# Kernel optimization log

Measured on AMD Instinct MI355X. Metric: run time of the kernel, lower is better.

## Reference

```python
import jax, jax.numpy as jnp
import numpy as np

NUM_HEADS = 12


def _rope(t, cos, sin):
    # t: (B, H, M, D); cos/sin: (M, D//2) applied to interleaved pairs
    B, H, M, D = t.shape
    t2 = t.reshape(B, H, M, D // 2, 2)
    t0, t1 = t2[..., 0], t2[..., 1]
    c = cos[None, None]  # (1,1,M,D//2)
    s = sin[None, None]
    r0 = t0 * c - t1 * s
    r1 = t0 * s + t1 * c
    return jnp.stack([r0, r1], axis=-1).reshape(B, H, M, D)


def setup_inputs() -> dict:
    key = jax.random.key(0)
    ks = jax.random.split(key, 7)
    B, N, C = 16, 577, 768
    Hd = C // NUM_HEADS
    x = jax.random.normal(ks[0], (B, N, C), dtype=jnp.float32)
    # rotary angles for N-1 non-CLS tokens
    theta = jax.random.uniform(ks[1], (N - 1, Hd // 2), dtype=jnp.float32) * 6.28318
    cos = jnp.cos(theta)
    sin = jnp.sin(theta)
    w_qkv = jax.random.normal(ks[2], (C, 3 * C), dtype=jnp.float32) * 0.02
    b_qkv = jax.random.normal(ks[3], (3 * C,), dtype=jnp.float32) * 0.02
    w_proj = jax.random.normal(ks[4], (C, C), dtype=jnp.float32) * 0.02
    b_proj = jax.random.normal(ks[5], (C,), dtype=jnp.float32) * 0.02
    return {"x": x, "cos": cos, "sin": sin, "w_qkv": w_qkv, "b_qkv": b_qkv,
            "w_proj": w_proj, "b_proj": b_proj}


def reference(x, cos, sin, w_qkv, b_qkv, w_proj, b_proj):
    B, N, C = x.shape
    H = NUM_HEADS
    D = C // H
    scale = D ** -0.5
    qkv = x @ w_qkv + b_qkv                       # (B, N, 3C)
    qkv = qkv.reshape(B, N, 3, H, D).transpose(2, 0, 3, 1, 4)  # (3, B, H, N, D)
    q, k, v = qkv[0], qkv[1], qkv[2]
    # RoPE applied to all tokens except the CLS token (index 0)
    q = jnp.concatenate([q[:, :, :1], _rope(q[:, :, 1:], cos, sin)], axis=2)
    k = jnp.concatenate([k[:, :, :1], _rope(k[:, :, 1:], cos, sin)], axis=2)
    attn = jax.nn.softmax(jnp.einsum('bhnd,bhmd->bhnm', q, k) * scale, axis=-1)
    out = jnp.einsum('bhnm,bhmd->bhnd', attn, v)  # (B, H, N, D)
    out = out.transpose(0, 2, 1, 3).reshape(B, N, C)
    return out @ w_proj + b_proj
```

## Files before the change

kernel.cpp:

```cpp
#include <hip/hip_runtime.h>
#include <stdint.h>

typedef unsigned short u16;
typedef __attribute__((ext_vector_type(8))) short bf16x8;
typedef __attribute__((ext_vector_type(4))) float f32x4;

#define MFMA16(a, b, c) __builtin_amdgcn_mfma_f32_16x16x32_bf16((a), (b), (c), 0, 0, 0)

__device__ __forceinline__ float b2f(u16 u) {
    union { unsigned int i; float f; } v; v.i = ((unsigned int)u) << 16; return v.f;
}
__device__ __forceinline__ u16 f2b(float f) {
    union { float f; unsigned int i; } v; v.f = f;
    unsigned int r = v.i + 0x7fffu + ((v.i >> 16) & 1u);
    return (u16)(r >> 16);
}
__device__ __forceinline__ float exp2_fast(float x) {
    float r; __asm__("v_exp_f32 %0, %1" : "=v"(r) : "v"(x)); return r;
}

typedef __attribute__((address_space(1))) void gvoid;
typedef __attribute__((address_space(3))) void lvoid;
__device__ __forceinline__ void gld16(const void* g, void* l) {
    __builtin_amdgcn_global_load_lds((gvoid*)(void*)g, (lvoid*)l, 16, 0, 0);
}

__device__ __forceinline__ void tile_from_bid(int bid, int nTM, int nTN,
                                              int& rt, int& ct) {
    const int PW = 8;
    const int full = nTM / PW;
    const int per = PW * nTN;
    int p = bid / per;
    int pw = PW;
    int rem = bid - p * per;
    if (p >= full) { p = full; rem = bid - full * per; pw = nTM - full * PW; }
    const int c = rem / pw;
    const int r = rem - c * pw;
    rt = p * PW + r;
    ct = c;
}

__global__ __launch_bounds__(256) void prep(const float* __restrict__ x,
                                            u16* __restrict__ xb,
                                            const float* __restrict__ wqkv,
                                            const float* __restrict__ wproj,
                                            u16* __restrict__ outQ,
                                            u16* __restrict__ outP) {
    __shared__ float tile[32][33];
    const int t = threadIdx.x;
    int bid = blockIdx.x;
    if (bid < 6924) {
        const int i = (bid * 256 + t) * 4;
        if (i + 3 < 7090176) {
            const float4 v = *(const float4*)(x + i);
            ushort4 o;
            o.x = f2b(v.x); o.y = f2b(v.y); o.z = f2b(v.z); o.w = f2b(v.w);
            *(ushort4*)(xb + i) = o;
        }
        return;
    }
    bid -= 6924;
    int bx = bid % 96;
    const int by = bid / 96;
    const float* in; u16* out; int C;
    if (bx < 72) { in = wqkv; out = outQ; C = 2304; }
    else         { bx -= 72; in = wproj; out = outP; C = 768; }
    const int R = 768;
    const int r = t >> 3, c4 = (t & 7) * 4;
    const int ir = by * 32 + r, ic = bx * 32 + c4;
    const float4 v = *(const float4*)(in + (size_t)ir * C + ic);
    tile[r][c4 + 0] = v.x; tile[r][c4 + 1] = v.y;
    tile[r][c4 + 2] = v.z; tile[r][c4 + 3] = v.w;
    __syncthreads();
    const int orow = bx * 32 + r, ocol = by * 32 + c4;
    ushort4 o;
    o.x = f2b(tile[c4 + 0][r]); o.y = f2b(tile[c4 + 1][r]);
    o.z = f2b(tile[c4 + 2][r]); o.w = f2b(tile[c4 + 3][r]);
    *(ushort4*)(out + (size_t)orow * R + ocol) = o;
}

template <int EPI>
__global__ __launch_bounds__(512) void gemm_bt(const u16* __restrict__ A,
                                               const u16* __restrict__ Bt,
                                               const float* __restrict__ bias,
                                               void* __restrict__ Cv,
                                               const float* __restrict__ cosp,
                                               const float* __restrict__ sinp,
                                               u16* __restrict__ VtG,
                                               int M, int N, int K) {
    __shared__ __align__(16) u16 As0[128 * 64];
    __shared__ __align__(16) u16 As1[128 * 64];
    __shared__ __align__(16) u16 Bs0[128 * 64];
    __shared__ __align__(16) u16 Bs1[128 * 64];

    const int t = threadIdx.x;
    const int lane = t & 63;
    const int wave = t >> 6;
    const int l15 = lane & 15, quad = lane >> 4;
    const int wm = wave >> 2;
    const int wn = wave & 3;

    int rt, ct;
    tile_from_bid(blockIdx.y * gridDim.x + blockIdx.x, gridDim.x, gridDim.y, rt, ct);
    const int row0 = rt * 128;
    const int col0 = ct * 128;

    const f32x4 fz = {0.f, 0.f, 0.f, 0.f};
    f32x4 acc[4][2];
#pragma unroll
    for (int i = 0; i < 4; ++i)
#pragma unroll
        for (int j = 0; j < 2; ++j) acc[i][j] = fz;

    const u16* Ap[2];
    const u16* Bp[2];
    int off[2];
#pragma unroll
    for (int n = 0; n < 2; ++n) {
        const int g = t + n * 512;
        const int row = g >> 3;
        const int slot = (g & 7) ^ (row & 7);
        int ar = row0 + row; if (ar > M - 1) ar = M - 1;
        Ap[n] = A + (size_t)ar * K + slot * 8;
        Bp[n] = Bt + (size_t)(col0 + row) * K + slot * 8;
        off[n] = g * 8;
    }

#define STAGE(kt_, Ad, Bd) do {                                            \
        const int kb_ = (kt_) << 6;                                        \
        gld16(Ap[0] + kb_, (Ad) + off[0]);                                 \
        gld16(Ap[1] + kb_, (Ad) + off[1]);                                 \
        gld16(Bp[0] + kb_, (Bd) + off[0]);                                 \
        gld16(Bp[1] + kb_, (Bd) + off[1]);                                 \
    } while (0)

#define COMPUTE(Asb, Bsb) do {                                             \
        _Pragma("unroll")                                                  \
        for (int kk = 0; kk < 2; ++kk) {                                   \
            const int swk = ((kk * 4 + quad) ^ (l15 & 7)) * 8;             \
            bf16x8 af[4], bfr[2];                                          \
            _Pragma("unroll")                                              \
            for (int mi = 0; mi < 4; ++mi)                                 \
                af[mi] = *(const bf16x8*)((Asb) +                          \
                    ((wm * 4 + mi) * 16 + l15) * 64 + swk);                \
            _Pragma("unroll")                                              \
            for (int ni = 0; ni < 2; ++ni)                                 \
                bfr[ni] = *(const bf16x8*)((Bsb) +                         \
                    ((wn * 2 + ni) * 16 + l15) * 64 + swk);                \
            _Pragma("unroll")                                              \
            for (int mi = 0; mi < 4; ++mi)                                 \
                _Pragma("unroll")                                          \
                for (int ni = 0; ni < 2; ++ni)                             \
                    acc[mi][ni] = MFMA16(bfr[ni], af[mi], acc[mi][ni]);    \
        }                                                                  \
    } while (0)

    const int nKT = K >> 6;
    STAGE(0, As0, Bs0);
    __syncthreads();

    for (int kt = 0; kt < nKT; kt += 2) {
        if (kt + 1 < nKT) STAGE(kt + 1, As1, Bs1);
        COMPUTE(As0, Bs0);
        __syncthreads();
        if (kt + 2 < nKT) STAGE(kt + 2, As0, Bs0);
        COMPUTE(As1, Bs1);
        __syncthreads();
    }
#undef STAGE
#undef COMPUTE

    if (EPI == 2) {
        if (col0 >= 1536) {
#pragma unroll
            for (int mi = 0; mi < 4; ++mi) {
                const int row = row0 + wm * 64 + mi * 16 + l15;
                if (row < M) {
                    const int bb = row / 577, n = row - bb * 577;
                    u16* vdst = VtG + (size_t)bb * 491520 + n;
#pragma unroll
                    for (int ni = 0; ni < 2; ++ni) {
                        const int colb = col0 + wn * 32 + ni * 16 + quad * 4;
                        const float4 bv = *(const float4*)(bias + colb);
#pragma unroll
                        for (int r = 0; r < 4; ++r) {
                            const int cv = colb + r - 1536;
                            vdst[(size_t)(cv >> 6) * 40960 + (cv & 63) * 640] =
                                f2b(acc[mi][ni][r] + ((const float*)&bv)[r]);
                        }
                    }
                }
            }
        } else {
#pragma unroll
            for (int mi = 0; mi < 4; ++mi) {
                const int row = row0 + wm * 64 + mi * 16 + l15;
                if (row < M) {
                    const int bb = row / 577, n = row - bb * 577;
                    const bool hr = (n >= 1);
                    const float* cb = cosp + (size_t)(hr ? (n - 1) : 0) * 32;
                    const float* sb = sinp + (size_t)(hr ? (n - 1) : 0) * 32;
                    u16* outp = (u16*)Cv + (size_t)row * 1536;
#pragma unroll
                    for (int ni = 0; ni < 2; ++ni) {
                        const int colb = col0 + wn * 32 + ni * 16 + quad * 4;
                        const float4 bv = *(const float4*)(bias + colb);
                        const int pi = (colb & 63) >> 1;
                        float2 c = *(const float2*)(cb + pi);
                        float2 s = *(const float2*)(sb + pi);
                        if (!hr) { c.x = 1.f; c.y = 1.f; s.x = 0.f; s.y = 0.f; }
                        const float v0 = acc[mi][ni][0] + bv.x;
                        const float v1 = acc[mi][ni][1] + bv.y;
                        const float v2 = acc[mi][ni][2] + bv.z;
                        const float v3 = acc[mi][ni][3] + bv.w;
                        ushort4 o;
                        o.x = f2b(v0 * c.x - v1 * s.x);
                        o.y = f2b(v0 * s.x + v1 * c.x);
                        o.z = f2b(v2 * c.y - v3 * s.y);
                        o.w = f2b(v2 * s.y + v3 * c.y);
                        *(ushort4*)(outp + colb) = o;
                    }
                }
            }
        }
    } else {
#pragma unroll
        for (int ni = 0; ni < 2; ++ni) {
            const int colb = col0 + wn * 32 + ni * 16 + quad * 4;
            const float4 bv = *(const float4*)(bias + colb);
#pragma unroll
            for (int mi = 0; mi < 4; ++mi) {
                const int row = row0 + wm * 64 + mi * 16 + l15;
                if (row < M) {
                    float4 o;
                    o.x = acc[mi][ni][0] + bv.x; o.y = acc[mi][ni][1] + bv.y;
                    o.z = acc[mi][ni][2] + bv.z; o.w = acc[mi][ni][3] + bv.w;
                    *(float4*)((float*)Cv + (size_t)row * N + colb) = o;
                }
            }
        }
    }
}

#define PSTR 72
#define CEXP 0.18033688011112042f

__global__ __launch_bounds__(512, 8) void attn2(const u16* __restrict__ qkv,
                                                const u16* __restrict__ VtG,
                                                u16* __restrict__ aout) {
    __shared__ __align__(16) u16 Ks[64 * 64];
    __shared__ __align__(16) u16 Vs[64 * 64];
    __shared__ __align__(16) u16 Pb[8 * 16 * PSTR];

    const int t = threadIdx.x;
    const int lane = t & 63, wave = t >> 6;
    const int l15 = lane & 15, quad = lane >> 4;

    const int bid = blockIdx.x;
    const int swz = (bid & 7) * 120 + (bid >> 3);
    const int bh = swz / 5, qt = swz - bh * 5;
    const int b = bh / 12, h = bh - b * 12;
    const u16* baseQ = qkv + (size_t)b * 577 * 1536 + h * 64;
    const u16* baseK = baseQ + 768;
    const u16* vbase = VtG + (size_t)bh * 64 * 640;

    const int mq = qt * 128 + wave * 16 + l15;
    const int nq = mq < 577 ? mq : 576;
    bf16x8 aq[2];
    aq[0] = *(const bf16x8*)(baseQ + (size_t)nq * 1536 + quad * 8);
    aq[1] = *(const bf16x8*)(baseQ + (size_t)nq * 1536 + 32 + quad * 8);

    const int r0 = t >> 3;
    const int s0 = (t & 7) ^ (r0 & 7);
    const int o0 = t * 8;
    const u16* Kp = baseK + (size_t)r0 * 1536 + s0 * 8;
    const u16* Vp = vbase + (size_t)r0 * 640 + s0 * 8;

    const int swk0 = (quad ^ (l15 & 7)) * 8;
    const int swk1 = ((4 + quad) ^ (l15 & 7)) * 8;

    u16* Pw = Pb + wave * 16 * PSTR;

    f32x4 oacc[4];
    const f32x4 fz = {0.f, 0.f, 0.f, 0.f};
#pragma unroll
    for (int i = 0; i < 4; ++i) oacc[i] = fz;
    float m1 = -1e30f;
    float l1 = 0.f;

#define ATT_TILE(kt_, MASKED) do {                                          \
        f32x4 sacc[4];                                                      \
        _Pragma("unroll")                                                   \
        for (int nt = 0; nt < 4; ++nt) {                                    \
            sacc[nt] = fz;                                                  \
            const bf16x8 bk0 = *(const bf16x8*)(Ks + (nt * 16 + l15) * 64 + swk0); \
            sacc[nt] = MFMA16(bk0, aq[0], sacc[nt]);                        \
            const bf16x8 bk1 = *(const bf16x8*)(Ks + (nt * 16 + l15) * 64 + swk1); \
            sacc[nt] = MFMA16(bk1, aq[1], sacc[nt]);                        \
        }                                                                   \
        if (MASKED) {                                                       \
            _Pragma("unroll")                                               \
            for (int nt = 0; nt < 4; ++nt)                                  \
                _Pragma("unroll")                                           \
                for (int r = 0; r < 4; ++r)                                 \
                    if (nt * 16 + quad * 4 + r > 0) sacc[nt][r] = -1e30f;   \
        }                                                                   \
        float mA = fmaxf(fmaxf(sacc[0][0], sacc[0][1]), fmaxf(sacc[0][2], sacc[0][3])); \
        float mB = fmaxf(fmaxf(sacc[1][0], sacc[1][1]), fmaxf(sacc[1][2], sacc[1][3])); \
        float mC = fmaxf(fmaxf(sacc[2][0], sacc[2][1]), fmaxf(sacc[2][2], sacc[2][3])); \
        float mD = fmaxf(fmaxf(sacc[3][0], sacc[3][1]), fmaxf(sacc[3][2], sacc[3][3])); \
        float mt = fmaxf(fmaxf(mA, mB), fmaxf(mC, mD));                     \
        mt = fmaxf(mt, __shfl_xor(mt, 16));                                 \
        mt = fmaxf(mt, __shfl_xor(mt, 32));                                 \
        const float mnew = fmaxf(m1, mt);                                   \
        const float alpha = exp2_fast((m1 - mnew) * CEXP);                  \
        m1 = mnew;                                                          \
        const float nmc = -mnew * CEXP;                                     \
        float lsum = 0.f;                                                   \
        _Pragma("unroll")                                                   \
        for (int nt = 0; nt < 4; ++nt) {                                    \
            const float p0 = exp2_fast(__builtin_fmaf(sacc[nt][0], CEXP, nmc)); \
            const float p1 = exp2_fast(__builtin_fmaf(sacc[nt][1], CEXP, nmc)); \
            const float p2 = exp2_fast(__builtin_fmaf(sacc[nt][2], CEXP, nmc)); \
            const float p3 = exp2_fast(__builtin_fmaf(sacc[nt][3], CEXP, nmc)); \
            lsum += (p0 + p1) + (p2 + p3);                                  \
            ushort4 pk;                                                     \
            pk.x = f2b(p0); pk.y = f2b(p1); pk.z = f2b(p2); pk.w = f2b(p3); \
            *(ushort4*)(Pw + l15 * PSTR + nt * 16 + quad * 4) = pk;         \
        }                                                                   \
        _Pragma("unroll")                                                   \
        for (int dt = 0; dt < 4; ++dt) {                                    \
            oacc[dt][0] *= alpha; oacc[dt][1] *= alpha;                     \
            oacc[dt][2] *= alpha; oacc[dt][3] *= alpha;                     \
        }                                                                   \
        __asm__ __volatile__("s_waitcnt lgkmcnt(0)" ::: "memory");          \
        _Pragma("unroll")                                                   \
        for (int kc = 0; kc < 2; ++kc) {                                    \
            const bf16x8 pf = *(const bf16x8*)(Pw + l15 * PSTR + kc * 32 + quad * 8); \
            const int swkv = kc ? swk1 : swk0;                              \
            _Pragma("unroll")                                               \
            for (int dt = 0; dt < 4; ++dt) {                                \
                const bf16x8 vf = *(const bf16x8*)(Vs + (dt * 16 + l15) * 64 + swkv); \
                oacc[dt] = MFMA16(vf, pf, oacc[dt]);                        \
            }                                                               \
        }                                                                   \
        lsum += __shfl_xor(lsum, 16);                                       \
        lsum += __shfl_xor(lsum, 32);                                       \
        l1 = l1 * alpha + lsum;                                             \
    } while (0)

    for (int kt = 0; kt < 9; ++kt) {
        gld16(Kp + (size_t)kt * 98304, Ks + o0);
        gld16(Vp + kt * 64, Vs + o0);
        __syncthreads();
        ATT_TILE(kt, false);
        __syncthreads();
    }
    gld16(baseK + (size_t)576 * 1536 + s0 * 8, Ks + o0);
    gld16(Vp + 576, Vs + o0);
    __syncthreads();
    ATT_TILE(9, true);

#undef ATT_TILE

    const int n = qt * 128 + wave * 16 + l15;
    if (n < 577) {
        const float linv = 1.f / l1;
        u16* op = aout + ((size_t)b * 577 + n) * 768 + h * 64 + quad * 4;
#pragma unroll
        for (int dt = 0; dt < 4; ++dt) {
            ushort4 o;
            o.x = f2b(oacc[dt][0] * linv); o.y = f2b(oacc[dt][1] * linv);
            o.z = f2b(oacc[dt][2] * linv); o.w = f2b(oacc[dt][3] * linv);
            *(ushort4*)(op + dt * 16) = o;
        }
    }
}

extern "C" void kernel_launch(void* const* d_in, const int* in_sizes, int n_in,
                              void* d_out, int out_size, void* d_ws, size_t ws_size,
                              hipStream_t stream) {
    const float* x      = (const float*)d_in[0];
    const float* cosp   = (const float*)d_in[1];
    const float* sinp   = (const float*)d_in[2];
    const float* w_qkv  = (const float*)d_in[3];
    const float* b_qkv  = (const float*)d_in[4];
    const float* w_proj = (const float*)d_in[5];
    const float* b_proj = (const float*)d_in[6];
    float* out = (float*)d_out;

    char* ws = (char*)d_ws;
    u16* xb     = (u16*)(ws);
    u16* aout   = (u16*)(ws);
    u16* wqkvT  = (u16*)(ws + 14180352);
    u16* wprojT = (u16*)(ws + 17719296);
    u16* qkv    = (u16*)(ws + 18898944);
    u16* VtG    = (u16*)(ws + 47259648);

    prep<<<9228, 256, 0, stream>>>(x, xb, w_qkv, w_proj, wqkvT, wprojT);
    gemm_bt<2><<<dim3(73, 18), 512, 0, stream>>>(xb, wqkvT, b_qkv, qkv,
                                                 cosp, sinp, VtG, 9232, 2304, 768);
    attn2<<<dim3(960), 512, 0, stream>>>(qkv, VtG, aout);
    gemm_bt<1><<<dim3(73, 6), 512, 0, stream>>>(aout, wprojT, b_proj, out,
                                                nullptr, nullptr, nullptr, 9232, 768, 768);
}
```

Before: 212.5 us.

## Use 256x128 single-buffered tile for QKV GEMM with fused RoPE/V-transpose epilogue

Splits the templated GEMM into a dedicated QKV kernel with a 256x128 block tile, a 4x4 MFMA fragment per wave (2x4 wave grid), and a simple single-buffered LDS loop. The grouped tile-ordering width becomes a parameter, set to 4 for the QKV GEMM. The goal is more arithmetic per LDS load and fewer blocks (666 instead of 1314), cutting global and LDS traffic for the largest GEMM. The cost is losing the double-buffered load/compute overlap, higher register pressure from 16 accumulators, and fewer blocks to spread across the CUs.

```diff
diff --git a/kernel.cpp b/kernel.cpp
--- a/kernel.cpp
+++ b/kernel.cpp
@@ -25,9 +25,8 @@
     __builtin_amdgcn_global_load_lds((gvoid*)(void*)g, (lvoid*)l, 16, 0, 0);
 }
 
-__device__ __forceinline__ void tile_from_bid(int bid, int nTM, int nTN,
+__device__ __forceinline__ void tile_from_bid(int bid, int nTM, int nTN, int PW,
                                               int& rt, int& ct) {
-    const int PW = 8;
     const int full = nTM / PW;
     const int per = PW * nTN;
     int p = bid / per;
@@ -79,15 +78,144 @@
     *(ushort4*)(out + (size_t)orow * R + ocol) = o;
 }
 
-template <int EPI>
-__global__ __launch_bounds__(512) void gemm_bt(const u16* __restrict__ A,
-                                               const u16* __restrict__ Bt,
-                                               const float* __restrict__ bias,
-                                               void* __restrict__ Cv,
-                                               const float* __restrict__ cosp,
-                                               const float* __restrict__ sinp,
-                                               u16* __restrict__ VtG,
-                                               int M, int N, int K) {
+__global__ __launch_bounds__(512) void gemm1k(const u16* __restrict__ A,
+                                              const u16* __restrict__ Bt,
+                                              const float* __restrict__ bias,
+                                              u16* __restrict__ qkv,
+                                              const float* __restrict__ cosp,
+                                              const float* __restrict__ sinp,
+                                              u16* __restrict__ VtG,
+                                              int M, int N, int K) {
+    __shared__ __align__(16) u16 As[256 * 64];
+    __shared__ __align__(16) u16 Bs[128 * 64];
+
+    const int t = threadIdx.x;
+    const int lane = t & 63;
+    const int wave = t >> 6;
+    const int l15 = lane & 15, quad = lane >> 4;
+    const int wm = wave >> 1;
+    const int wn = wave & 1;
+
+    int rt, ct;
+    tile_from_bid(blockIdx.y * gridDim.x + blockIdx.x, gridDim.x, gridDim.y, 4, rt, ct);
+    const int row0 = rt * 256;
+    const int col0 = ct * 128;
+
+    const f32x4 fz = {0.f, 0.f, 0.f, 0.f};
+    f32x4 acc[4][4];
+#pragma unroll
+    for (int i = 0; i < 4; ++i)
+#pragma unroll
+        for (int j = 0; j < 4; ++j) acc[i][j] = fz;
+
+    const u16* Ap[4]; int offA[4];
+    const u16* Bp[2]; int offB[2];
+#pragma unroll
+    for (int n = 0; n < 4; ++n) {
+        const int g = t + n * 512;
+        const int row = g >> 3;
+        const int slot = (g & 7) ^ (row & 7);
+        int ar = row0 + row; if (ar > M - 1) ar = M - 1;
+        Ap[n] = A + (size_t)ar * K + slot * 8;
+        offA[n] = g * 8;
+    }
+#pragma unroll
+    for (int n = 0; n < 2; ++n) {
+        const int g = t + n * 512;
+        const int row = g >> 3;
+        const int slot = (g & 7) ^ (row & 7);
+        Bp[n] = Bt + (size_t)(col0 + row) * K + slot * 8;
+        offB[n] = g * 8;
+    }
+
+    const int nKT = K >> 6;
+    for (int kt = 0; kt < nKT; ++kt) {
+        const int kb = kt << 6;
+        gld16(Ap[0] + kb, As + offA[0]);
+        gld16(Ap[1] + kb, As + offA[1]);
+        gld16(Ap[2] + kb, As + offA[2]);
+        gld16(Ap[3] + kb, As + offA[3]);
+        gld16(Bp[0] + kb, Bs + offB[0]);
+        gld16(Bp[1] + kb, Bs + offB[1]);
+        __syncthreads();
+#pragma unroll
+        for (int kk = 0; kk < 2; ++kk) {
+            const int swk = ((kk * 4 + quad) ^ (l15 & 7)) * 8;
+            bf16x8 af[4], bfr[4];
+#pragma unroll
+            for (int mi = 0; mi < 4; ++mi)
+                af[mi] = *(const bf16x8*)(As + ((wm * 4 + mi) * 16 + l15) * 64 + swk);
+#pragma unroll
+            for (int ni = 0; ni < 4; ++ni)
+                bfr[ni] = *(const bf16x8*)(Bs + ((wn * 4 + ni) * 16 + l15) * 64 + swk);
+#pragma unroll
+            for (int mi = 0; mi < 4; ++mi)
+#pragma unroll
+                for (int ni = 0; ni < 4; ++ni)
+                    acc[mi][ni] = MFMA16(bfr[ni], af[mi], acc[mi][ni]);
+        }
+        __syncthreads();
+    }
+
+    if (col0 >= 1536) {
+#pragma unroll
+        for (int mi = 0; mi < 4; ++mi) {
+            const int row = row0 + wm * 64 + mi * 16 + l15;
+            if (row < M) {
+                const int bb = row / 577, n = row - bb * 577;
+                u16* vdst = VtG + (size_t)bb * 491520 + n;
+#pragma unroll
+                for (int ni = 0; ni < 4; ++ni) {
+                    const int colb = col0 + wn * 64 + ni * 16 + quad * 4;
+                    const float4 bv = *(const float4*)(bias + colb);
+#pragma unroll
+                    for (int r = 0; r < 4; ++r) {
+                        const int cv = colb + r - 1536;
+                        vdst[(size_t)(cv >> 6) * 40960 + (cv & 63) * 640] =
+                            f2b(acc[mi][ni][r] + ((const float*)&bv)[r]);
+                    }
+                }
+            }
+        }
+    } else {
+#pragma unroll
+        for (int mi = 0; mi < 4; ++mi) {
+            const int row = row0 + wm * 64 + mi * 16 + l15;
+            if (row < M) {
+                const int bb = row / 577, n = row - bb * 577;
+                const bool hr = (n >= 1);
+                const float* cb = cosp + (size_t)(hr ? (n - 1) : 0) * 32;
+                const float* sb = sinp + (size_t)(hr ? (n - 1) : 0) * 32;
+                u16* outp = qkv + (size_t)row * 1536;
+#pragma unroll
+                for (int ni = 0; ni < 4; ++ni) {
+                    const int colb = col0 + wn * 64 + ni * 16 + quad * 4;
+                    const float4 bv = *(const float4*)(bias + colb);
+                    const int pi = (colb & 63) >> 1;
+                    float2 c = *(const float2*)(cb + pi);
+                    float2 s = *(const float2*)(sb + pi);
+                    if (!hr) { c.x = 1.f; c.y = 1.f; s.x = 0.f; s.y = 0.f; }
+                    const float v0 = acc[mi][ni][0] + bv.x;
+                    const float v1 = acc[mi][ni][1] + bv.y;
+                    const float v2 = acc[mi][ni][2] + bv.z;
+                    const float v3 = acc[mi][ni][3] + bv.w;
+                    ushort4 o;
+                    o.x = f2b(v0 * c.x - v1 * s.x);
+                    o.y = f2b(v0 * s.x + v1 * c.x);
+                    o.z = f2b(v2 * c.y - v3 * s.y);
+                    o.w = f2b(v2 * s.y + v3 * c.y);
+                    *(ushort4*)(outp + colb) = o;
+                }
+            }
+        }
+    }
+}
+
+__global__ __launch_bounds__(512) void gemm2k(const u16* __restrict__ A,
+                                              const u16* __restrict__ Bt,
+                                              const float* __restrict__ bias,
+                                              float* __restrict__ C,
+                                              int M, int N, int K) {
     __shared__ __align__(16) u16 As0[128 * 64];
     __shared__ __align__(16) u16 As1[128 * 64];
     __shared__ __align__(16) u16 Bs0[128 * 64];
@@ -101,7 +229,7 @@
     const int wn = wave & 3;
 
     int rt, ct;
-    tile_from_bid(blockIdx.y * gridDim.x + blockIdx.x, gridDim.x, gridDim.y, rt, ct);
+    tile_from_bid(blockIdx.y * gridDim.x + blockIdx.x, gridDim.x, gridDim.y, 8, rt, ct);
     const int row0 = rt * 128;
     const int col0 = ct * 128;
 
@@ -170,73 +298,18 @@
 #undef STAGE
 #undef COMPUTE
 
-    if (EPI == 2) {
-        if (col0 >= 1536) {
-#pragma unroll
-            for (int mi = 0; mi < 4; ++mi) {
-                const int row = row0 + wm * 64 + mi * 16 + l15;
-                if (row < M) {
-                    const int bb = row / 577, n = row - bb * 577;
-                    u16* vdst = VtG + (size_t)bb * 491520 + n;
-#pragma unroll
-                    for (int ni = 0; ni < 2; ++ni) {
-                        const int colb = col0 + wn * 32 + ni * 16 + quad * 4;
-                        const float4 bv = *(const float4*)(bias + colb);
-#pragma unroll
-                        for (int r = 0; r < 4; ++r) {
-                            const int cv = colb + r - 1536;
-                            vdst[(size_t)(cv >> 6) * 40960 + (cv & 63) * 640] =
-                                f2b(acc[mi][ni][r] + ((const float*)&bv)[r]);
-                        }
-                    }
-                }
-            }
-        } else {
-#pragma unroll
-            for (int mi = 0; mi < 4; ++mi) {
-                const int row = row0 + wm * 64 + mi * 16 + l15;
-                if (row < M) {
-                    const int bb = row / 577, n = row - bb * 577;
-                    const bool hr = (n >= 1);
-                    const float* cb = cosp + (size_t)(hr ? (n - 1) : 0) * 32;
-                    const float* sb = sinp + (size_t)(hr ? (n - 1) : 0) * 32;
-                    u16* outp = (u16*)Cv + (size_t)row * 1536;
-#pragma unroll
-                    for (int ni = 0; ni < 2; ++ni) {
-                        const int colb = col0 + wn * 32 + ni * 16 + quad * 4;
-                        const float4 bv = *(const float4*)(bias + colb);
-                        const int pi = (colb & 63) >> 1;
-                        float2 c = *(const float2*)(cb + pi);
-                        float2 s = *(const float2*)(sb + pi);
-                        if (!hr) { c.x = 1.f; c.y = 1.f; s.x = 0.f; s.y = 0.f; }
-                        const float v0 = acc[mi][ni][0] + bv.x;
-                        const float v1 = acc[mi][ni][1] + bv.y;
-                        const float v2 = acc[mi][ni][2] + bv.z;
-                        const float v3 = acc[mi][ni][3] + bv.w;
-                        ushort4 o;
-                        o.x = f2b(v0 * c.x - v1 * s.x);
-                        o.y = f2b(v0 * s.x + v1 * c.x);
-                        o.z = f2b(v2 * c.y - v3 * s.y);
-                        o.w = f2b(v2 * s.y + v3 * c.y);
-                        *(ushort4*)(outp + colb) = o;
-                    }
-                }
-            }
-        }
-    } else {
-#pragma unroll
-        for (int ni = 0; ni < 2; ++ni) {
-            const int colb = col0 + wn * 32 + ni * 16 + quad * 4;
-            const float4 bv = *(const float4*)(bias + colb);
-#pragma unroll
-            for (int mi = 0; mi < 4; ++mi) {
-                const int row = row0 + wm * 64 + mi * 16 + l15;
-                if (row < M) {
-                    float4 o;
-                    o.x = acc[mi][ni][0] + bv.x; o.y = acc[mi][ni][1] + bv.y;
-                    o.z = acc[mi][ni][2] + bv.z; o.w = acc[mi][ni][3] + bv.w;
-                    *(float4*)((float*)Cv + (size_t)row * N + colb) = o;
-                }
+#pragma unroll
+    for (int ni = 0; ni < 2; ++ni) {
+        const int colb = col0 + wn * 32 + ni * 16 + quad * 4;
+        const float4 bv = *(const float4*)(bias + colb);
+#pragma unroll
+        for (int mi = 0; mi < 4; ++mi) {
+            const int row = row0 + wm * 64 + mi * 16 + l15;
+            if (row < M) {
+                float4 o;
+                o.x = acc[mi][ni][0] + bv.x; o.y = acc[mi][ni][1] + bv.y;
+                o.z = acc[mi][ni][2] + bv.z; o.w = acc[mi][ni][3] + bv.w;
+                *(float4*)(C + (size_t)row * N + colb) = o;
             }
         }
     }
@@ -398,9 +471,9 @@
     u16* VtG    = (u16*)(ws + 47259648);
 
     prep<<<9228, 256, 0, stream>>>(x, xb, w_qkv, w_proj, wqkvT, wprojT);
-    gemm_bt<2><<<dim3(73, 18), 512, 0, stream>>>(xb, wqkvT, b_qkv, qkv,
-                                                 cosp, sinp, VtG, 9232, 2304, 768);
+    gemm1k<<<dim3(37, 18), 512, 0, stream>>>(xb, wqkvT, b_qkv, qkv,
+                                             cosp, sinp, VtG, 9232, 2304, 768);
     attn2<<<dim3(960), 512, 0, stream>>>(qkv, VtG, aout);
-    gemm_bt<1><<<dim3(73, 6), 512, 0, stream>>>(aout, wprojT, b_proj, out,
-                                                nullptr, nullptr, nullptr, 9232, 768, 768);
-}
+    gemm2k<<<dim3(73, 6), 512, 0, stream>>>(aout, wprojT, b_proj, out,
+                                            9232, 768, 768);
+}
```

Result: no change. 213.6 us (+0.5%).
